# Performance work log

Measured on AMD Instinct MI355X. Metric: run time of the kernel, lower is better.

The kernel has to match this reference:

```python
import jax, jax.numpy as jnp
import numpy as np

NUM_HEADS = 16
ROPE_BASE = 10000.0

def rotate_half(x):
    h = x.shape[-1] // 2
    return jnp.concatenate([-x[..., h:], x[..., :h]], axis=-1)

def rope_cos_sin(seq_len, head_dim, dtype):
    inv_freq = 1.0 / (ROPE_BASE ** (jnp.arange(0, head_dim, 2, dtype=jnp.float32) / head_dim))
    t = jnp.arange(seq_len, dtype=jnp.float32)
    freqs = jnp.outer(t, inv_freq)              # [N, hd/2]
    emb = jnp.concatenate([freqs, freqs], -1)   # [N, hd]
    return jnp.cos(emb).astype(dtype), jnp.sin(emb).astype(dtype)

def setup_inputs() -> dict:
    key = jax.random.key(0)
    ks = jax.random.split(key, 5)
    B, N, D = 2, 2048, 1024
    s = 1.0 / np.sqrt(D)
    return {
        "x": jax.random.normal(ks[0], (B, N, D), jnp.float32),
        "attention_mask": jnp.ones((B, N), jnp.int32),
        "Wq": jax.random.normal(ks[1], (D, D), jnp.float32) * s,
        "Wk": jax.random.normal(ks[2], (D, D), jnp.float32) * s,
        "Wv": jax.random.normal(ks[3], (D, D), jnp.float32) * s,
        "Wo": jax.random.normal(ks[4], (D, D), jnp.float32) * s,
    }

def reference(x, attention_mask, Wq, Wk, Wv, Wo):
    B, N, D = x.shape
    H = NUM_HEADS
    hd = D // H
    scale = hd ** -0.5
    # projections (nn.Linear: x @ W.T), split heads -> [B, H, N, hd]
    q = jnp.einsum('bnd,ed->bne', x, Wq).reshape(B, N, H, hd).transpose(0, 2, 1, 3)
    k = jnp.einsum('bnd,ed->bne', x, Wk).reshape(B, N, H, hd).transpose(0, 2, 1, 3)
    v = jnp.einsum('bnd,ed->bne', x, Wv).reshape(B, N, H, hd).transpose(0, 2, 1, 3)
    cos, sin = rope_cos_sin(N, hd, x.dtype)     # [N, hd]
    cos = cos[None, None]; sin = sin[None, None]
    q = q * cos + rotate_half(q) * sin
    k = k * cos + rotate_half(k) * sin
    attn = jnp.einsum('bhqd,bhkd->bhqk', q, k) * scale
    mask = attention_mask.astype(bool)[:, None, None, :]        # [B,1,1,N]
    attn = jnp.where(mask, attn, -jnp.inf)
    all_masked = (attention_mask.sum(-1) == 0)[:, None, None, None]
    attn = jnp.where(all_masked, 0.0, attn)
    attn = jax.nn.softmax(attn, axis=-1)
    out = jnp.einsum('bhqk,bhkd->bhqd', attn, v)
    out = out.transpose(0, 2, 1, 3).reshape(B, N, D)
    return jnp.einsum('bnd,ed->bne', out, Wo)
```

## Files before the change

kernel.cpp:

```cpp
#include <hip/hip_runtime.h>
#include <math.h>

#define BATCH 2
#define SEQ   2048
#define DM    1024
#define NH    16
#define HD    64
#define MTOT  (BATCH*SEQ)

typedef short v8s __attribute__((ext_vector_type(8)));
typedef short v4s __attribute__((ext_vector_type(4)));
typedef float v4f __attribute__((ext_vector_type(4)));

#define MFMA16(a, b, c) __builtin_amdgcn_mfma_f32_16x16x32_bf16((a), (b), (c), 0, 0, 0)

__device__ __forceinline__ short f2b(float f) {
    union { float f; unsigned u; } v; v.f = f;
    return (short)((v.u + 0x8000u) >> 16);
}

__device__ __forceinline__ void rope_cs(int n, float f_rev, float* c, float* s) {
    float rev = (float)n * f_rev;
    float t = rev - floorf(rev);
    float ang = t * 6.283185307179586f;
    *c = __cosf(ang);
    *s = __sinf(ang);
}

#define L2_1E4_D32 0.4152410118609203f
#define INV2PI     0.15915494309189535f
#define QSCALE     0.18033688011112042f

__global__ __launch_bounds__(256) void cvt_all_kernel(
    const float* __restrict__ x,  const float* __restrict__ wq,
    const float* __restrict__ wk, const float* __restrict__ wv,
    const float* __restrict__ wo, short* __restrict__ dst)
{
    int i = blockIdx.x * 256 + threadIdx.x;
    const float* src; int off;
    if (i < (1 << 19)) { src = x; off = i; }
    else {
        int j = i - (1 << 19);
        int wsel = j >> 17;
        off = j & ((1 << 17) - 1);
        src = (wsel == 0) ? wq : (wsel == 1) ? wk : (wsel == 2) ? wv : wo;
    }
    const float4* s4 = (const float4*)src;
    float4 a = s4[2 * off], b = s4[2 * off + 1];
    v8s p;
    p[0] = f2b(a.x); p[1] = f2b(a.y); p[2] = f2b(a.z); p[3] = f2b(a.w);
    p[4] = f2b(b.x); p[5] = f2b(b.y); p[6] = f2b(b.z); p[7] = f2b(b.w);
    *(v8s*)&dst[8 * i] = p;
}

__global__ __launch_bounds__(256, 3) void qkv_rope_mfma(
    const short* __restrict__ xb, const short* __restrict__ Wqb,
    const short* __restrict__ Wkb, const short* __restrict__ Wvb,
    short* __restrict__ K, short* __restrict__ Vt, short* __restrict__ Qb)
{
    const int zz = blockIdx.z;
    const short* __restrict__ Wb = (zz == 0) ? Wkb : (zz == 1) ? Wvb : Wqb;
    const int m0 = blockIdx.x * 128, e00 = blockIdx.y * 128;
    const int tid = threadIdx.x;
    const int w = tid >> 6, lane = tid & 63, lq = lane >> 4, lr = lane & 15;
    const int wm = w >> 1, wn = w & 1;

    __shared__ union {
        struct { short As[128][32]; short Bs[128][32]; } p1;
        short Css[128][136];
    } u;

    v4f acc[4][4];
    #pragma unroll
    for (int i = 0; i < 4; ++i)
        for (int j = 0; j < 4; ++j)
            for (int r = 0; r < 4; ++r) acc[i][j][r] = 0.f;

    const int arow = tid >> 1, aseg = (tid & 1) * 16;
    for (int k0 = 0; k0 < DM; k0 += 32) {
        v8s a0 = *(const v8s*)&xb[(size_t)(m0 + arow) * DM + k0 + aseg];
        v8s a1 = *(const v8s*)&xb[(size_t)(m0 + arow) * DM + k0 + aseg + 8];
        v8s b0 = *(const v8s*)&Wb[(size_t)(e00 + arow) * DM + k0 + aseg];
        v8s b1 = *(const v8s*)&Wb[(size_t)(e00 + arow) * DM + k0 + aseg + 8];
        __syncthreads();
        *(v8s*)&u.p1.As[arow][aseg] = a0;
        *(v8s*)&u.p1.As[arow][aseg + 8] = a1;
        *(v8s*)&u.p1.Bs[arow][aseg] = b0;
        *(v8s*)&u.p1.Bs[arow][aseg + 8] = b1;
        __syncthreads();
        v8s af[4], bf[4];
        #pragma unroll
        for (int i = 0; i < 4; ++i)
            af[i] = *(const v8s*)&u.p1.As[64 * wm + 16 * i + lr][8 * lq];
        #pragma unroll
        for (int j = 0; j < 4; ++j)
            bf[j] = *(const v8s*)&u.p1.Bs[64 * wn + 16 * j + lr][8 * lq];
        #pragma unroll
        for (int i = 0; i < 4; ++i)
            #pragma unroll
            for (int j = 0; j < 4; ++j)
                acc[i][j] = MFMA16(af[i], bf[j], acc[i][j]);
    }
    __syncthreads();

    const int b = m0 >> 11, n00 = m0 & (SEQ - 1);

    if (zz != 1) {
        short* __restrict__ dst = (zz == 0) ? K : Qb;
        const float sc = (zz == 0) ? 1.0f : QSCALE;
        float f0 = exp2f(-(float)lr * L2_1E4_D32) * INV2PI;
        float f1 = exp2f(-(float)(16 + lr) * L2_1E4_D32) * INV2PI;
        #pragma unroll
        for (int i = 0; i < 4; ++i) {
            #pragma unroll
            for (int r = 0; r < 4; ++r) {
                int row = 64 * wm + 16 * i + 4 * lq + r;
                int n = n00 + row;
                float c0v, s0v, c1v, s1v;
                rope_cs(n, f0, &c0v, &s0v);
                rope_cs(n, f1, &c1v, &s1v);
                float q0 = acc[i][0][r], q1 = acc[i][1][r];
                float q2 = acc[i][2][r], q3 = acc[i][3][r];
                u.Css[row][64 * wn + lr]      = f2b(sc * (q0 * c0v - q2 * s0v));
                u.Css[row][64 * wn + 16 + lr] = f2b(sc * (q1 * c1v - q3 * s1v));
                u.Css[row][64 * wn + 32 + lr] = f2b(sc * (q2 * c0v + q0 * s0v));
                u.Css[row][64 * wn + 48 + lr] = f2b(sc * (q3 * c1v + q1 * s1v));
            }
        }
        __syncthreads();
        int row = tid >> 1, hh = tid & 1;
        int h = (e00 >> 6) + hh;
        int n = n00 + row;
        size_t base = (((size_t)(b * NH + h)) * SEQ + n) * HD;
        #pragma unroll
        for (int p = 0; p < 8; ++p)
            *(v8s*)&dst[base + 8 * p] = *(const v8s*)&u.Css[row][64 * hh + 8 * p];
    } else {
        #pragma unroll
        for (int i = 0; i < 4; ++i) {
            #pragma unroll
            for (int j = 0; j < 4; ++j) {
                v4s t;
                #pragma unroll
                for (int r = 0; r < 4; ++r) t[r] = f2b(acc[i][j][r]);
                *(v4s*)&u.Css[64 * wn + 16 * j + lr][64 * wm + 16 * i + 4 * lq] = t;
            }
        }
        __syncthreads();
        int c = tid >> 1, half = (tid & 1) * 64;
        int h = (e00 + c) >> 6, d = (e00 + c) & 63;
        size_t base = (((size_t)(b * NH + h)) * HD + d) * SEQ + n00 + half;
        #pragma unroll
        for (int p = 0; p < 8; ++p)
            *(v8s*)&Vt[base + 8 * p] = *(const v8s*)&u.Css[c][half + 8 * p];
    }
}

__global__ __launch_bounds__(512, 4) void attn_mfma(
    const short* __restrict__ Qb, const short* __restrict__ K,
    const short* __restrict__ Vt, const int* __restrict__ mask,
    short* __restrict__ O)
{
    const int m0 = blockIdx.x * 128, h = blockIdx.y;
    const int b = m0 >> 11, n0 = m0 & (SEQ - 1), bh = b * NH + h;
    const int tid = threadIdx.x;
    const int w = tid >> 6, lane = tid & 63, lq = lane >> 4, lr = lane & 15;

    __shared__ short Ks[128][72];
    __shared__ short Vs[64][136];
    __shared__ short Ps[128][72];
    __shared__ float mbias[128];

    const short* __restrict__ Qh = Qb + (size_t)bh * SEQ * HD;
    v8s aq[2];
    #pragma unroll
    for (int ks = 0; ks < 2; ++ks)
        aq[ks] = *(const v8s*)&Qh[(size_t)(n0 + 16 * w + lr) * HD + 32 * ks + 8 * lq];

    float lacc[4] = {0.f, 0.f, 0.f, 0.f};
    v4f o[4];
    #pragma unroll
    for (int nt = 0; nt < 4; ++nt)
        for (int r = 0; r < 4; ++r) o[nt][r] = 0.f;

    const int kr = tid >> 2, kc = (tid & 3) * 16;
    const int krh = kr & 63;
    const int pkr = 64 * (kr >> 6) + 16 * (krh & 3) + (krh >> 2);
    const int vr = tid >> 3, vc = (tid & 7) * 16;
    const short* __restrict__ Kb = K + (size_t)bh * SEQ * HD;
    const short* __restrict__ Vb = Vt + (size_t)bh * HD * SEQ;

    v8s k1 = *(const v8s*)&Kb[(size_t)kr * HD + kc];
    v8s k2 = *(const v8s*)&Kb[(size_t)kr * HD + kc + 8];
    v8s v1 = *(const v8s*)&Vb[(size_t)vr * SEQ + vc];
    v8s v2 = *(const v8s*)&Vb[(size_t)vr * SEQ + vc + 8];
    int mnext = (tid < 128) ? mask[b * SEQ + tid] : 0;

    for (int c0 = 0; c0 < SEQ; c0 += 128) {
        __syncthreads();
        *(v8s*)&Ks[pkr][kc] = k1;
        *(v8s*)&Ks[pkr][kc + 8] = k2;
        *(v8s*)&Vs[vr][vc] = v1;
        *(v8s*)&Vs[vr][vc + 8] = v2;
        if (tid < 128) mbias[tid] = mnext ? -24.0f : -1e30f;
        __syncthreads();
        if (c0 + 128 < SEQ) {
            k1 = *(const v8s*)&Kb[(size_t)(c0 + 128 + kr) * HD + kc];
            k2 = *(const v8s*)&Kb[(size_t)(c0 + 128 + kr) * HD + kc + 8];
            v1 = *(const v8s*)&Vb[(size_t)vr * SEQ + c0 + 128 + vc];
            v2 = *(const v8s*)&Vb[(size_t)vr * SEQ + c0 + 128 + vc + 8];
            if (tid < 128) mnext = mask[b * SEQ + c0 + 128 + tid];
        }

        #pragma unroll
        for (int half = 0; half < 2; ++half) {
            v8s kf[2][4];
            #pragma unroll
            for (int ks = 0; ks < 2; ++ks)
                #pragma unroll
                for (int nt = 0; nt < 4; ++nt)
                    kf[ks][nt] = *(const v8s*)&Ks[64 * half + 16 * nt + lr][32 * ks + 8 * lq];
            float bias[4];
            #pragma unroll
            for (int nt = 0; nt < 4; ++nt) bias[nt] = mbias[64 * half + 4 * lr + nt];

            v4f sv[4];
            #pragma unroll
            for (int nt = 0; nt < 4; ++nt)
                for (int r = 0; r < 4; ++r) sv[nt][r] = 0.f;
            #pragma unroll
            for (int ks = 0; ks < 2; ++ks)
                #pragma unroll
                for (int nt = 0; nt < 4; ++nt)
                    sv[nt] = MFMA16(aq[ks], kf[ks][nt], sv[nt]);

            #pragma unroll
            for (int r = 0; r < 4; ++r) {
                v4s pk;
                #pragma unroll
                for (int nt = 0; nt < 4; ++nt) {
                    float p = exp2f(sv[nt][r] + bias[nt]);
                    lacc[r] += p;
                    pk[nt] = f2b(p);
                }
                *(v4s*)&Ps[16 * w + 4 * lq + r][4 * lr] = pk;
            }
            #pragma unroll
            for (int ks = 0; ks < 2; ++ks) {
                v8s a = *(const v8s*)&Ps[16 * w + lr][32 * ks + 8 * lq];
                #pragma unroll
                for (int nt = 0; nt < 4; ++nt) {
                    v8s vf = *(const v8s*)&Vs[16 * nt + lr][64 * half + 32 * ks + 8 * lq];
                    o[nt] = MFMA16(a, vf, o[nt]);
                }
            }
        }
    }

    #pragma unroll
    for (int r = 0; r < 4; ++r) {
        float l = lacc[r];
        l += __shfl_xor(l, 1);
        l += __shfl_xor(l, 2);
        l += __shfl_xor(l, 4);
        l += __shfl_xor(l, 8);
        float inv = (l > 0.f) ? 1.f / l : 0.f;
        int qrow = 16 * w + 4 * lq + r;
        #pragma unroll
        for (int nt = 0; nt < 4; ++nt)
            O[(size_t)(m0 + qrow) * DM + h * HD + 16 * nt + lr] =
                f2b(o[nt][r] * inv);
    }
}

__global__ __launch_bounds__(256, 2) void oproj_mfma(
    const short* __restrict__ O, const short* __restrict__ Wob,
    float* __restrict__ out)
{
    const int m0 = blockIdx.x * 64, e00 = blockIdx.y * 128;
    const int tid = threadIdx.x;
    const int w = tid >> 6, lane = tid & 63, lq = lane >> 4, lr = lane & 15;

    __shared__ short As[64][32];
    __shared__ short Bs[128][32];

    v4f acc[4][2];
    #pragma unroll
    for (int i = 0; i < 4; ++i)
        for (int j = 0; j < 2; ++j)
            for (int r = 0; r < 4; ++r) acc[i][j][r] = 0.f;

    const int arow = tid >> 2, aseg = (tid & 3) * 8;
    const int brow = tid >> 1, bseg = (tid & 1) * 16;
    for (int k0 = 0; k0 < DM; k0 += 32) {
        v8s a0 = *(const v8s*)&O[(size_t)(m0 + arow) * DM + k0 + aseg];
        v8s b0 = *(const v8s*)&Wob[(size_t)(e00 + brow) * DM + k0 + bseg];
        v8s b1 = *(const v8s*)&Wob[(size_t)(e00 + brow) * DM + k0 + bseg + 8];
        __syncthreads();
        *(v8s*)&As[arow][aseg] = a0;
        *(v8s*)&Bs[brow][bseg] = b0;
        *(v8s*)&Bs[brow][bseg + 8] = b1;
        __syncthreads();
        v8s af[4], bf[2];
        #pragma unroll
        for (int i = 0; i < 4; ++i)
            af[i] = *(const v8s*)&As[16 * i + lr][8 * lq];
        #pragma unroll
        for (int j = 0; j < 2; ++j)
            bf[j] = *(const v8s*)&Bs[32 * w + 16 * j + lr][8 * lq];
        #pragma unroll
        for (int i = 0; i < 4; ++i)
            #pragma unroll
            for (int j = 0; j < 2; ++j)
                acc[i][j] = MFMA16(af[i], bf[j], acc[i][j]);
    }

    #pragma unroll
    for (int i = 0; i < 4; ++i)
        #pragma unroll
        for (int r = 0; r < 4; ++r) {
            int m = m0 + 16 * i + 4 * lq + r;
            #pragma unroll
            for (int j = 0; j < 2; ++j)
                out[(size_t)m * DM + e00 + 32 * w + 16 * j + lr] = acc[i][j][r];
        }
}

extern "C" void kernel_launch(void* const* d_in, const int* in_sizes, int n_in,
                              void* d_out, int out_size, void* d_ws, size_t ws_size,
                              hipStream_t stream)
{
    const float* x    = (const float*)d_in[0];
    const int*   mask = (const int*)d_in[1];
    const float* Wq   = (const float*)d_in[2];
    const float* Wk   = (const float*)d_in[3];
    const float* Wv   = (const float*)d_in[4];
    const float* Wo   = (const float*)d_in[5];
    float* out = (float*)d_out;

    short* xb  = (short*)d_ws;
    short* Wqb = xb  + (size_t)MTOT * DM;
    short* Wkb = Wqb + (size_t)DM * DM;
    short* Wvb = Wkb + (size_t)DM * DM;
    short* Wob = Wvb + (size_t)DM * DM;
    short* Qb  = Wob + (size_t)DM * DM;
    short* O   = xb;
    short* K  = (short*)d_out;
    short* Vt = K + (size_t)MTOT * DM;

    cvt_all_kernel<<<4096, 256, 0, stream>>>(x, Wq, Wk, Wv, Wo, xb);

    dim3 g1(MTOT / 128, DM / 128, 3);
    qkv_rope_mfma<<<g1, 256, 0, stream>>>(xb, Wqb, Wkb, Wvb, K, Vt, Qb);

    dim3 g2(MTOT / 128, NH);
    attn_mfma<<<g2, 512, 0, stream>>>(Qb, K, Vt, mask, O);

    dim3 g3(MTOT / 64, DM / 128);
    oproj_mfma<<<g3, 256, 0, stream>>>(O, Wob, out);
}
```

Before: 211.1 us.

## Use direct global-to-LDS loads in GEMMs and tighten attention softmax path

The QKV and output-projection GEMMs now stage tiles with global_load_lds (16-byte direct-to-LDS loads) instead of loading through registers and then writing to shared memory. In the attention kernel, the mask bias is moved into the padding column of the K tile, replacing the separate mbias array. The exp2 and bf16 packing now use inline v_exp_f32 and v_cvt_pk_bf16_f32 instructions. The occupancy hint rises from 4 to 6 blocks per SM, which may force register spills.

```diff
diff --git a/kernel.cpp b/kernel.cpp
--- a/kernel.cpp
+++ b/kernel.cpp
@@ -17,6 +17,16 @@
 __device__ __forceinline__ short f2b(float f) {
     union { float f; unsigned u; } v; v.f = f;
     return (short)((v.u + 0x8000u) >> 16);
+}
+
+__device__ __forceinline__ float fexp2(float x) {
+    float r; asm("v_exp_f32 %0, %1" : "=v"(r) : "v"(x)); return r;
+}
+
+__device__ __forceinline__ void gload16(const void* g, void* lds) {
+    __builtin_amdgcn_global_load_lds(
+        (const __attribute__((address_space(1))) void*)g,
+        (__attribute__((address_space(3))) void*)lds, 16, 0, 0);
 }
 
 __device__ __forceinline__ void rope_cs(int n, float f_rev, float* c, float* s) {
@@ -76,17 +86,13 @@
         for (int j = 0; j < 4; ++j)
             for (int r = 0; r < 4; ++r) acc[i][j][r] = 0.f;
 
-    const int arow = tid >> 1, aseg = (tid & 1) * 16;
+    const int gr = lane >> 2, gc = 8 * (lane & 3);
     for (int k0 = 0; k0 < DM; k0 += 32) {
-        v8s a0 = *(const v8s*)&xb[(size_t)(m0 + arow) * DM + k0 + aseg];
-        v8s a1 = *(const v8s*)&xb[(size_t)(m0 + arow) * DM + k0 + aseg + 8];
-        v8s b0 = *(const v8s*)&Wb[(size_t)(e00 + arow) * DM + k0 + aseg];
-        v8s b1 = *(const v8s*)&Wb[(size_t)(e00 + arow) * DM + k0 + aseg + 8];
-        __syncthreads();
-        *(v8s*)&u.p1.As[arow][aseg] = a0;
-        *(v8s*)&u.p1.As[arow][aseg + 8] = a1;
-        *(v8s*)&u.p1.Bs[arow][aseg] = b0;
-        *(v8s*)&u.p1.Bs[arow][aseg + 8] = b1;
+        __syncthreads();
+        gload16(&xb[(size_t)(m0 + 32 * w      + gr) * DM + k0 + gc], &u.p1.As[32 * w][0]);
+        gload16(&xb[(size_t)(m0 + 32 * w + 16 + gr) * DM + k0 + gc], &u.p1.As[32 * w + 16][0]);
+        gload16(&Wb[(size_t)(e00 + 32 * w      + gr) * DM + k0 + gc], &u.p1.Bs[32 * w][0]);
+        gload16(&Wb[(size_t)(e00 + 32 * w + 16 + gr) * DM + k0 + gc], &u.p1.Bs[32 * w + 16][0]);
         __syncthreads();
         v8s af[4], bf[4];
         #pragma unroll
@@ -156,7 +162,7 @@
     }
 }
 
-__global__ __launch_bounds__(512, 4) void attn_mfma(
+__global__ __launch_bounds__(512, 6) void attn_mfma(
     const short* __restrict__ Qb, const short* __restrict__ K,
     const short* __restrict__ Vt, const int* __restrict__ mask,
     short* __restrict__ O)
@@ -169,7 +175,6 @@
     __shared__ short Ks[128][72];
     __shared__ short Vs[64][136];
     __shared__ short Ps[128][72];
-    __shared__ float mbias[128];
 
     const short* __restrict__ Qh = Qb + (size_t)bh * SEQ * HD;
     v8s aq[2];
@@ -194,7 +199,7 @@
     v8s k2 = *(const v8s*)&Kb[(size_t)kr * HD + kc + 8];
     v8s v1 = *(const v8s*)&Vb[(size_t)vr * SEQ + vc];
     v8s v2 = *(const v8s*)&Vb[(size_t)vr * SEQ + vc + 8];
-    int mnext = (tid < 128) ? mask[b * SEQ + tid] : 0;
+    int mnext = ((tid & 3) == 0) ? mask[b * SEQ + (tid >> 2)] : 0;
 
     for (int c0 = 0; c0 < SEQ; c0 += 128) {
         __syncthreads();
@@ -202,14 +207,14 @@
         *(v8s*)&Ks[pkr][kc + 8] = k2;
         *(v8s*)&Vs[vr][vc] = v1;
         *(v8s*)&Vs[vr][vc + 8] = v2;
-        if (tid < 128) mbias[tid] = mnext ? -24.0f : -1e30f;
+        if ((tid & 3) == 0) *(float*)&Ks[pkr][64] = mnext ? -24.0f : -1e30f;
         __syncthreads();
         if (c0 + 128 < SEQ) {
             k1 = *(const v8s*)&Kb[(size_t)(c0 + 128 + kr) * HD + kc];
             k2 = *(const v8s*)&Kb[(size_t)(c0 + 128 + kr) * HD + kc + 8];
             v1 = *(const v8s*)&Vb[(size_t)vr * SEQ + c0 + 128 + vc];
             v2 = *(const v8s*)&Vb[(size_t)vr * SEQ + c0 + 128 + vc + 8];
-            if (tid < 128) mnext = mask[b * SEQ + c0 + 128 + tid];
+            if ((tid & 3) == 0) mnext = mask[b * SEQ + c0 + 128 + (tid >> 2)];
         }
 
         #pragma unroll
@@ -222,7 +227,8 @@
                     kf[ks][nt] = *(const v8s*)&Ks[64 * half + 16 * nt + lr][32 * ks + 8 * lq];
             float bias[4];
             #pragma unroll
-            for (int nt = 0; nt < 4; ++nt) bias[nt] = mbias[64 * half + 4 * lr + nt];
+            for (int nt = 0; nt < 4; ++nt)
+                bias[nt] = *(const float*)&Ks[64 * half + 16 * nt + lr][64];
 
             v4f sv[4];
             #pragma unroll
@@ -236,14 +242,16 @@
 
             #pragma unroll
             for (int r = 0; r < 4; ++r) {
-                v4s pk;
-                #pragma unroll
-                for (int nt = 0; nt < 4; ++nt) {
-                    float p = exp2f(sv[nt][r] + bias[nt]);
-                    lacc[r] += p;
-                    pk[nt] = f2b(p);
-                }
-                *(v4s*)&Ps[16 * w + 4 * lq + r][4 * lr] = pk;
+                float p0 = fexp2(sv[0][r] + bias[0]);
+                float p1 = fexp2(sv[1][r] + bias[1]);
+                float p2 = fexp2(sv[2][r] + bias[2]);
+                float p3 = fexp2(sv[3][r] + bias[3]);
+                lacc[r] += (p0 + p1) + (p2 + p3);
+                unsigned u0, u1;
+                asm("v_cvt_pk_bf16_f32 %0, %1, %2" : "=v"(u0) : "v"(p0), "v"(p1));
+                asm("v_cvt_pk_bf16_f32 %0, %1, %2" : "=v"(u1) : "v"(p2), "v"(p3));
+                uint2 pk; pk.x = u0; pk.y = u1;
+                *(uint2*)&Ps[16 * w + 4 * lq + r][4 * lr] = pk;
             }
             #pragma unroll
             for (int ks = 0; ks < 2; ++ks) {
@@ -290,16 +298,12 @@
         for (int j = 0; j < 2; ++j)
             for (int r = 0; r < 4; ++r) acc[i][j][r] = 0.f;
 
-    const int arow = tid >> 2, aseg = (tid & 3) * 8;
-    const int brow = tid >> 1, bseg = (tid & 1) * 16;
+    const int gr = lane >> 2, gc = 8 * (lane & 3);
     for (int k0 = 0; k0 < DM; k0 += 32) {
-        v8s a0 = *(const v8s*)&O[(size_t)(m0 + arow) * DM + k0 + aseg];
-        v8s b0 = *(const v8s*)&Wob[(size_t)(e00 + brow) * DM + k0 + bseg];
-        v8s b1 = *(const v8s*)&Wob[(size_t)(e00 + brow) * DM + k0 + bseg + 8];
-        __syncthreads();
-        *(v8s*)&As[arow][aseg] = a0;
-        *(v8s*)&Bs[brow][bseg] = b0;
-        *(v8s*)&Bs[brow][bseg + 8] = b1;
+        __syncthreads();
+        gload16(&O[(size_t)(m0 + 16 * w + gr) * DM + k0 + gc],         &As[16 * w][0]);
+        gload16(&Wob[(size_t)(e00 + 32 * w      + gr) * DM + k0 + gc], &Bs[32 * w][0]);
+        gload16(&Wob[(size_t)(e00 + 32 * w + 16 + gr) * DM + k0 + gc], &Bs[32 * w + 16][0]);
         __syncthreads();
         v8s af[4], bf[2];
         #pragma unroll
```

Result: slower. 263.6 us (+24.9%).
